# Kernel tuning notes

Hardware: AMD Instinct MI355X
Metric: run time of the kernel (lower is better)

The kernel has to match this reference:

```python
import jax, jax.numpy as jnp
import numpy as np

B, D, H = 8192, 1024, 1024

def setup_inputs() -> dict:
    key = jax.random.key(0)
    ks = jax.random.split(key, 7)
    s_x = 1.0 / np.sqrt(D)
    s_h = 1.0 / np.sqrt(H)
    return {
        "e_t": jax.random.normal(ks[0], (B, D), jnp.float32),
        "h_prev": jax.random.normal(ks[1], (B, H), jnp.float32),
        "c_prev": jax.random.normal(ks[2], (B, H), jnp.float32),
        # gates concatenated in order (f, i, o, c), each block of size H
        "W_x": jax.random.uniform(ks[3], (4 * H, D), jnp.float32, -s_x, s_x),
        "b_x": jax.random.uniform(ks[4], (4 * H,), jnp.float32, -s_x, s_x),
        "W_h": jax.random.uniform(ks[5], (4 * H, H), jnp.float32, -s_h, s_h),
        "b_h": jax.random.uniform(ks[6], (4 * H,), jnp.float32, -s_h, s_h),
        "b_extra": jnp.zeros((4 * H,), jnp.float32),  # the b_f/b_i/b_o/b_c Parameters
    }

def reference(e_t, h_prev, c_prev, W_x, b_x, W_h, b_h, b_extra):
    # two fused GEMMs: [B,D]@[D,4H] and [B,H]@[H,4H]
    z = (jnp.einsum('bd,gd->bg', e_t, W_x)
         + jnp.einsum('bh,gh->bg', h_prev, W_h)
         + b_x + b_h + b_extra)  # [B, 4H]
    zf, zi, zo, zc = jnp.split(z, 4, axis=-1)
    g_t = jax.nn.sigmoid(zf)   # forget gate
    p_t = jax.nn.sigmoid(zi)   # input gate
    q_t = jax.nn.sigmoid(zo)   # output gate
    m_t_hat = jnp.tanh(zc)     # candidate cell
    c_t = g_t * c_prev + p_t * m_t_hat
    h_t = q_t * jnp.tanh(c_t)
    return (h_t, c_t)
```

## Files before the change

kernel.cpp:

```cpp
#include <hip/hip_runtime.h>
#include <stdint.h>

#define B_ROWS 8192
#define DH     1024
#define KTOT   2048
#define NTOT   4096

typedef __attribute__((ext_vector_type(8))) __bf16 bf16x8;
typedef __attribute__((ext_vector_type(4))) float  f32x4;

__device__ __forceinline__ unsigned short f2bf(float f) {
    unsigned int u = __float_as_uint(f);
    u += 0x7FFFu + ((u >> 16) & 1u);
    return (unsigned short)(u >> 16);
}

__device__ __forceinline__ float fast_sigmoid(float x) {
    return 1.0f / (1.0f + __expf(-x));
}
__device__ __forceinline__ float fast_tanh(float x) {
    float e = __expf(fminf(-2.0f * x, 80.0f));
    return (1.0f - e) / (1.0f + e);
}
__device__ __forceinline__ float sel4(float g0, float g1, float g2, float g3, int u) {
    float r = g0;
    r = (u == 1) ? g1 : r;
    r = (u == 2) ? g2 : r;
    r = (u == 3) ? g3 : r;
    return r;
}

#define NBLK_A (B_ROWS)
#define NBLK_W (NTOT)
#define NBLK_BIAS (NTOT / 256)

__global__ __launch_bounds__(256) void pack_all(const float* __restrict__ e_t,
                                                const float* __restrict__ h_prev,
                                                const float* __restrict__ W_x,
                                                const float* __restrict__ W_h,
                                                const float* __restrict__ b_x,
                                                const float* __restrict__ b_h,
                                                const float* __restrict__ b_e,
                                                unsigned short* __restrict__ A_cat,
                                                unsigned short* __restrict__ W_cat,
                                                float* __restrict__ bias) {
    const int blk = blockIdx.x;
    const int t   = threadIdx.x;
    if (blk < NBLK_A + NBLK_W) {
        const float* src0;
        unsigned short* dst;
        int row;
        if (blk < NBLK_A) {
            row = blk;
            dst = A_cat + (size_t)row * KTOT;
            int c8 = t << 3;
            src0 = (c8 < DH) ? (e_t + (size_t)row * DH + c8)
                             : (h_prev + (size_t)row * DH + (c8 - DH));
        } else {
            row = blk - NBLK_A;
            int h = row >> 2, gate = row & 3;
            int srow = gate * DH + h;
            dst = W_cat + (size_t)row * KTOT;
            int c8 = t << 3;
            src0 = (c8 < DH) ? (W_x + (size_t)srow * DH + c8)
                             : (W_h + (size_t)srow * DH + (c8 - DH));
        }
        float4 f0 = ((const float4*)src0)[0];
        float4 f1 = ((const float4*)src0)[1];
        uint4 o;
        o.x = (unsigned)f2bf(f0.x) | ((unsigned)f2bf(f0.y) << 16);
        o.y = (unsigned)f2bf(f0.z) | ((unsigned)f2bf(f0.w) << 16);
        o.z = (unsigned)f2bf(f1.x) | ((unsigned)f2bf(f1.y) << 16);
        o.w = (unsigned)f2bf(f1.z) | ((unsigned)f2bf(f1.w) << 16);
        *(uint4*)(dst + t * 8) = o;
    } else {
        int gp = (blk - NBLK_A - NBLK_W) * 256 + t;
        int h = gp >> 2, gate = gp & 3;
        int g = gate * DH + h;
        bias[gp] = b_x[g] + b_h[g] + b_e[g];
    }
}


#define GLL(srcp, dstp) \
    __builtin_amdgcn_global_load_lds( \
        (const __attribute__((address_space(1))) void*)(srcp), \
        (__attribute__((address_space(3))) void*)(dstp), 16, 0, 0)

#define STAGE_HALF(g, buf, h, kt) do { \
    GLL((g) + ((size_t)((h) * 128)      * KTOT) + (size_t)(kt) * 64, (buf) + (((h) * 128)      + w8) * 128); \
    GLL((g) + ((size_t)((h) * 128 + 64) * KTOT) + (size_t)(kt) * 64, (buf) + (((h) * 128 + 64) + w8) * 128); \
} while (0)

#define PHASE_MID() do { \
    __builtin_amdgcn_sched_barrier(0); \
    __builtin_amdgcn_s_barrier(); \
    asm volatile("s_waitcnt lgkmcnt(0)" ::: "memory"); \
    __builtin_amdgcn_sched_barrier(0); \
} while (0)

#define PHASE_END() do { \
    __builtin_amdgcn_sched_barrier(0); \
    __builtin_amdgcn_s_barrier(); \
    __builtin_amdgcn_sched_barrier(0); \
} while (0)

template <int MODE>
__device__ __forceinline__ void do_tile(
    int kt,
    unsigned char* As_cur, unsigned char* Bs_cur,
    const unsigned short* __restrict__ gA, const unsigned short* __restrict__ gB,
    int w8, int rowA, int rowB, int xg0, int xg1,
    f32x4 (&acc)[8][4])
{
    bf16x8 afl[4][2], afh[4][2], bfl[2][2], bfh[2][2];

#pragma unroll
    for (int mi = 0; mi < 4; ++mi) {
        afl[mi][0] = *(const bf16x8*)(As_cur + rowA + mi * 2048 + xg0);
        afl[mi][1] = *(const bf16x8*)(As_cur + rowA + mi * 2048 + xg1);
    }
#pragma unroll
    for (int ni = 0; ni < 2; ++ni) {
        bfl[ni][0] = *(const bf16x8*)(Bs_cur + rowB + ni * 2048 + xg0);
        bfl[ni][1] = *(const bf16x8*)(Bs_cur + rowB + ni * 2048 + xg1);
    }
    PHASE_MID();
    __builtin_amdgcn_s_setprio(1);
#pragma unroll
    for (int mi = 0; mi < 4; ++mi)
#pragma unroll
        for (int ni = 0; ni < 2; ++ni) {
            acc[mi][ni] = __builtin_amdgcn_mfma_f32_16x16x32_bf16(afl[mi][0], bfl[ni][0], acc[mi][ni], 0, 0, 0);
            acc[mi][ni] = __builtin_amdgcn_mfma_f32_16x16x32_bf16(afl[mi][1], bfl[ni][1], acc[mi][ni], 0, 0, 0);
        }
    __builtin_amdgcn_s_setprio(0);
    PHASE_END();

#pragma unroll
    for (int ni = 0; ni < 2; ++ni) {
        bfh[ni][0] = *(const bf16x8*)(Bs_cur + rowB + (2 + ni) * 2048 + xg0);
        bfh[ni][1] = *(const bf16x8*)(Bs_cur + rowB + (2 + ni) * 2048 + xg1);
    }
    PHASE_MID();
    __builtin_amdgcn_s_setprio(1);
#pragma unroll
    for (int mi = 0; mi < 4; ++mi)
#pragma unroll
        for (int ni = 0; ni < 2; ++ni) {
            acc[mi][2 + ni] = __builtin_amdgcn_mfma_f32_16x16x32_bf16(afl[mi][0], bfh[ni][0], acc[mi][2 + ni], 0, 0, 0);
            acc[mi][2 + ni] = __builtin_amdgcn_mfma_f32_16x16x32_bf16(afl[mi][1], bfh[ni][1], acc[mi][2 + ni], 0, 0, 0);
        }
    __builtin_amdgcn_s_setprio(0);
    PHASE_END();

#pragma unroll
    for (int mi = 0; mi < 4; ++mi) {
        afh[mi][0] = *(const bf16x8*)(As_cur + rowA + (4 + mi) * 2048 + xg0);
        afh[mi][1] = *(const bf16x8*)(As_cur + rowA + (4 + mi) * 2048 + xg1);
    }
    if constexpr (MODE == 2) {
        STAGE_HALF(gB, Bs_cur, 0, kt + 2);
        STAGE_HALF(gB, Bs_cur, 1, kt + 2);
    }
    PHASE_MID();
    __builtin_amdgcn_s_setprio(1);
#pragma unroll
    for (int mi = 0; mi < 4; ++mi)
#pragma unroll
        for (int ni = 0; ni < 2; ++ni) {
            acc[4 + mi][ni] = __builtin_amdgcn_mfma_f32_16x16x32_bf16(afh[mi][0], bfl[ni][0], acc[4 + mi][ni], 0, 0, 0);
            acc[4 + mi][ni] = __builtin_amdgcn_mfma_f32_16x16x32_bf16(afh[mi][1], bfl[ni][1], acc[4 + mi][ni], 0, 0, 0);
        }
    __builtin_amdgcn_s_setprio(0);
    PHASE_END();

    if constexpr (MODE == 2) {
        STAGE_HALF(gA, As_cur, 0, kt + 2);
        STAGE_HALF(gA, As_cur, 1, kt + 2);
        __builtin_amdgcn_sched_barrier(0);
        asm volatile("s_waitcnt vmcnt(8)" ::: "memory");
        __builtin_amdgcn_sched_barrier(0);
    } else if constexpr (MODE == 1) {
        __builtin_amdgcn_sched_barrier(0);
        asm volatile("s_waitcnt vmcnt(0)" ::: "memory");
        __builtin_amdgcn_sched_barrier(0);
    }
    PHASE_MID();
    __builtin_amdgcn_s_setprio(1);
#pragma unroll
    for (int mi = 0; mi < 4; ++mi)
#pragma unroll
        for (int ni = 0; ni < 2; ++ni) {
            acc[4 + mi][2 + ni] = __builtin_amdgcn_mfma_f32_16x16x32_bf16(afh[mi][0], bfh[ni][0], acc[4 + mi][2 + ni], 0, 0, 0);
            acc[4 + mi][2 + ni] = __builtin_amdgcn_mfma_f32_16x16x32_bf16(afh[mi][1], bfh[ni][1], acc[4 + mi][2 + ni], 0, 0, 0);
        }
    __builtin_amdgcn_s_setprio(0);
    PHASE_END();
}

__global__ __launch_bounds__(512, 2) void lstm_gemm(
    const unsigned short* __restrict__ A,
    const unsigned short* __restrict__ Wc,
    const float* __restrict__ bias,
    const float* __restrict__ c_prev,
    float* __restrict__ h_out,
    float* __restrict__ c_out)
{
    __shared__ __align__(16) unsigned char lds[131072];

    const int tid = threadIdx.x;
    const int w   = tid >> 6;
    const int l   = tid & 63;
    const int wm  = w >> 2, wn = w & 3;
    const int m0  = blockIdx.y * 256;
    const int n0  = blockIdx.x * 256;
    const int w8  = w * 8;

    f32x4 acc[8][4];
#pragma unroll
    for (int i = 0; i < 8; ++i)
#pragma unroll
        for (int j = 0; j < 4; ++j) acc[i][j] = {0.f, 0.f, 0.f, 0.f};

    const int srow = w8 + (l >> 3);
    const int scol = ((l & 7) ^ ((l >> 3) & 7)) * 8;
    const unsigned short* gA = A  + (size_t)(m0 + srow) * KTOT + scol;
    const unsigned short* gB = Wc + (size_t)(n0 + srow) * KTOT + scol;

    unsigned char* As0 = lds;
    unsigned char* As1 = lds + 32768;
    unsigned char* Bs0 = lds + 65536;
    unsigned char* Bs1 = lds + 98304;

    const int lane15 = l & 15;
    const int quad   = l >> 4;
    const int rowA = (wm * 128 + lane15) * 128;
    const int rowB = (wn * 64  + lane15) * 128;
    const int xg0  = ((0 + quad) ^ (lane15 & 7)) * 16;
    const int xg1  = ((4 + quad) ^ (lane15 & 7)) * 16;

    STAGE_HALF(gA, As0, 0, 0);
    STAGE_HALF(gA, As0, 1, 0);
    STAGE_HALF(gB, Bs0, 0, 0);
    STAGE_HALF(gB, Bs0, 1, 0);
    STAGE_HALF(gA, As1, 0, 1);
    STAGE_HALF(gA, As1, 1, 1);
    STAGE_HALF(gB, Bs1, 0, 1);
    STAGE_HALF(gB, Bs1, 1, 1);
    asm volatile("s_waitcnt vmcnt(8)" ::: "memory");
    __builtin_amdgcn_s_barrier();

#pragma unroll 1
    for (int kt2 = 0; kt2 < 15; ++kt2) {
        do_tile<2>(2 * kt2,     As0, Bs0, gA, gB, w8, rowA, rowB, xg0, xg1, acc);
        do_tile<2>(2 * kt2 + 1, As1, Bs1, gA, gB, w8, rowA, rowB, xg0, xg1, acc);
    }
    do_tile<1>(30, As0, Bs0, gA, gB, w8, rowA, rowB, xg0, xg1, acc);
    do_tile<0>(31, As1, Bs1, gA, gB, w8, rowA, rowB, xg0, xg1, acc);

    float biasv[4];
#pragma unroll
    for (int nj = 0; nj < 4; ++nj)
        biasv[nj] = bias[n0 + wn * 64 + nj * 16 + lane15];

    const int u = (l >> 2) & 3;
    const int v = l & 3;
    const int src_base = (l & 0x30) | (v << 2);
    const int hbase = (n0 + wn * 64) >> 2;

#pragma unroll
    for (int mi = 0; mi < 8; ++mi) {
        const int m = m0 + wm * 128 + mi * 16 + quad * 4 + u;
#pragma unroll
        for (int nj = 0; nj < 4; ++nj) {
            f32x4 a = acc[mi][nj];
            float bb = biasv[nj];
            float a0 = a[0] + bb, a1 = a[1] + bb, a2 = a[2] + bb, a3 = a[3] + bb;

            float s0, s1, s2, s3;
            s0 = __shfl(a0, src_base | 0, 64); s1 = __shfl(a1, src_base | 0, 64);
            s2 = __shfl(a2, src_base | 0, 64); s3 = __shfl(a3, src_base | 0, 64);
            float zf = sel4(s0, s1, s2, s3, u);
            s0 = __shfl(a0, src_base | 1, 64); s1 = __shfl(a1, src_base | 1, 64);
            s2 = __shfl(a2, src_base | 1, 64); s3 = __shfl(a3, src_base | 1, 64);
            float zi = sel4(s0, s1, s2, s3, u);
            s0 = __shfl(a0, src_base | 2, 64); s1 = __shfl(a1, src_base | 2, 64);
            s2 = __shfl(a2, src_base | 2, 64); s3 = __shfl(a3, src_base | 2, 64);
            float zo = sel4(s0, s1, s2, s3, u);
            s0 = __shfl(a0, src_base | 3, 64); s1 = __shfl(a1, src_base | 3, 64);
            s2 = __shfl(a2, src_base | 3, 64); s3 = __shfl(a3, src_base | 3, 64);
            float zc = sel4(s0, s1, s2, s3, u);

            float gf = fast_sigmoid(zf);
            float gi = fast_sigmoid(zi);
            float go = fast_sigmoid(zo);
            float mh = fast_tanh(zc);

            const int h = hbase + nj * 4 + v;
            const size_t off = (size_t)m * DH + h;
            float cp = c_prev[off];
            float ct = gf * cp + gi * mh;
            float ht = go * fast_tanh(ct);
            h_out[off] = ht;
            c_out[off] = ct;
        }
    }
}

extern "C" void kernel_launch(void* const* d_in, const int* in_sizes, int n_in,
                              void* d_out, int out_size, void* d_ws, size_t ws_size,
                              hipStream_t stream) {
    const float* e_t     = (const float*)d_in[0];
    const float* h_prev  = (const float*)d_in[1];
    const float* c_prev  = (const float*)d_in[2];
    const float* W_x     = (const float*)d_in[3];
    const float* b_x     = (const float*)d_in[4];
    const float* W_h     = (const float*)d_in[5];
    const float* b_h     = (const float*)d_in[6];
    const float* b_extra = (const float*)d_in[7];

    float* h_out = (float*)d_out;
    float* c_out = h_out + (size_t)B_ROWS * DH;

    unsigned short* A_cat = (unsigned short*)d_ws;
    unsigned short* W_cat = (unsigned short*)((char*)d_ws + (size_t)B_ROWS * KTOT * 2);
    float*          bias  = (float*)((char*)d_ws + (size_t)B_ROWS * KTOT * 2 + (size_t)NTOT * KTOT * 2);

    pack_all<<<NBLK_A + NBLK_W + NBLK_BIAS, 256, 0, stream>>>(
        e_t, h_prev, W_x, W_h, b_x, b_h, b_extra, A_cat, W_cat, bias);
    lstm_gemm<<<dim3(NTOT / 256, B_ROWS / 256), 512, 0, stream>>>(
        A_cat, W_cat, bias, c_prev, h_out, c_out);
}
```

Baseline: 322.2 us.

## Regroup weight gate interleave by 16 and restructure LDS/MFMA phase synchronization

The packed weight and bias layout now interleaves gates in blocks of 16 columns instead of 4. Each lane's four accumulator fragments then hold f/i/o/c for the same hidden unit, so the epilogue's cross-lane shuffles and selects go away. The main loop issues all LDS fragment loads up front and uses counted lgkmcnt waits before each MFMA group. It also drops most of the per-phase workgroup barriers, keeping one before staging the next global-to-LDS loads and one at tile end. This cuts barrier stalls and shuffle overhead, at the risk of ordering hazards on reuse of the LDS buffers and higher register pressure.

```diff
diff --git a/kernel.cpp b/kernel.cpp
--- a/kernel.cpp
+++ b/kernel.cpp
@@ -21,13 +21,6 @@
 __device__ __forceinline__ float fast_tanh(float x) {
     float e = __expf(fminf(-2.0f * x, 80.0f));
     return (1.0f - e) / (1.0f + e);
-}
-__device__ __forceinline__ float sel4(float g0, float g1, float g2, float g3, int u) {
-    float r = g0;
-    r = (u == 1) ? g1 : r;
-    r = (u == 2) ? g2 : r;
-    r = (u == 3) ? g3 : r;
-    return r;
 }
 
 #define NBLK_A (B_ROWS)
@@ -58,7 +51,8 @@
                              : (h_prev + (size_t)row * DH + (c8 - DH));
         } else {
             row = blk - NBLK_A;
-            int h = row >> 2, gate = row & 3;
+            int gate = (row >> 4) & 3;
+            int h    = (row >> 6) * 16 + (row & 15);
             int srow = gate * DH + h;
             dst = W_cat + (size_t)row * KTOT;
             int c8 = t << 3;
@@ -75,8 +69,9 @@
         *(uint4*)(dst + t * 8) = o;
     } else {
         int gp = (blk - NBLK_A - NBLK_W) * 256 + t;
-        int h = gp >> 2, gate = gp & 3;
-        int g = gate * DH + h;
+        int gate = (gp >> 4) & 3;
+        int h    = (gp >> 6) * 16 + (gp & 15);
+        int g    = gate * DH + h;
         bias[gp] = b_x[g] + b_h[g] + b_e[g];
     }
 }
@@ -92,18 +87,7 @@
     GLL((g) + ((size_t)((h) * 128 + 64) * KTOT) + (size_t)(kt) * 64, (buf) + (((h) * 128 + 64) + w8) * 128); \
 } while (0)
 
-#define PHASE_MID() do { \
-    __builtin_amdgcn_sched_barrier(0); \
-    __builtin_amdgcn_s_barrier(); \
-    asm volatile("s_waitcnt lgkmcnt(0)" ::: "memory"); \
-    __builtin_amdgcn_sched_barrier(0); \
-} while (0)
-
-#define PHASE_END() do { \
-    __builtin_amdgcn_sched_barrier(0); \
-    __builtin_amdgcn_s_barrier(); \
-    __builtin_amdgcn_sched_barrier(0); \
-} while (0)
+#define SB() __builtin_amdgcn_sched_barrier(0)
 
 template <int MODE>
 __device__ __forceinline__ void do_tile(
@@ -125,7 +109,22 @@
         bfl[ni][0] = *(const bf16x8*)(Bs_cur + rowB + ni * 2048 + xg0);
         bfl[ni][1] = *(const bf16x8*)(Bs_cur + rowB + ni * 2048 + xg1);
     }
-    PHASE_MID();
+    SB();
+#pragma unroll
+    for (int ni = 0; ni < 2; ++ni) {
+        bfh[ni][0] = *(const bf16x8*)(Bs_cur + rowB + (2 + ni) * 2048 + xg0);
+        bfh[ni][1] = *(const bf16x8*)(Bs_cur + rowB + (2 + ni) * 2048 + xg1);
+    }
+    SB();
+#pragma unroll
+    for (int mi = 0; mi < 4; ++mi) {
+        afh[mi][0] = *(const bf16x8*)(As_cur + rowA + (4 + mi) * 2048 + xg0);
+        afh[mi][1] = *(const bf16x8*)(As_cur + rowA + (4 + mi) * 2048 + xg1);
+    }
+    SB();
+
+    asm volatile("s_waitcnt lgkmcnt(12)" ::: "memory");
+    SB();
     __builtin_amdgcn_s_setprio(1);
 #pragma unroll
     for (int mi = 0; mi < 4; ++mi)
@@ -135,14 +134,10 @@
             acc[mi][ni] = __builtin_amdgcn_mfma_f32_16x16x32_bf16(afl[mi][1], bfl[ni][1], acc[mi][ni], 0, 0, 0);
         }
     __builtin_amdgcn_s_setprio(0);
-    PHASE_END();
-
-#pragma unroll
-    for (int ni = 0; ni < 2; ++ni) {
-        bfh[ni][0] = *(const bf16x8*)(Bs_cur + rowB + (2 + ni) * 2048 + xg0);
-        bfh[ni][1] = *(const bf16x8*)(Bs_cur + rowB + (2 + ni) * 2048 + xg1);
-    }
-    PHASE_MID();
+    SB();
+
+    asm volatile("s_waitcnt lgkmcnt(8)" ::: "memory");
+    SB();
     __builtin_amdgcn_s_setprio(1);
 #pragma unroll
     for (int mi = 0; mi < 4; ++mi)
@@ -152,18 +147,20 @@
             acc[mi][2 + ni] = __builtin_amdgcn_mfma_f32_16x16x32_bf16(afl[mi][1], bfh[ni][1], acc[mi][2 + ni], 0, 0, 0);
         }
     __builtin_amdgcn_s_setprio(0);
-    PHASE_END();
-
-#pragma unroll
-    for (int mi = 0; mi < 4; ++mi) {
-        afh[mi][0] = *(const bf16x8*)(As_cur + rowA + (4 + mi) * 2048 + xg0);
-        afh[mi][1] = *(const bf16x8*)(As_cur + rowA + (4 + mi) * 2048 + xg1);
-    }
+    SB();
+
+    asm volatile("s_waitcnt lgkmcnt(0)" ::: "memory");
+    SB();
     if constexpr (MODE == 2) {
+        __builtin_amdgcn_s_barrier();
+        SB();
         STAGE_HALF(gB, Bs_cur, 0, kt + 2);
         STAGE_HALF(gB, Bs_cur, 1, kt + 2);
-    }
-    PHASE_MID();
+        STAGE_HALF(gA, As_cur, 0, kt + 2);
+        STAGE_HALF(gA, As_cur, 1, kt + 2);
+        SB();
+    }
+
     __builtin_amdgcn_s_setprio(1);
 #pragma unroll
     for (int mi = 0; mi < 4; ++mi)
@@ -173,20 +170,7 @@
             acc[4 + mi][ni] = __builtin_amdgcn_mfma_f32_16x16x32_bf16(afh[mi][1], bfl[ni][1], acc[4 + mi][ni], 0, 0, 0);
         }
     __builtin_amdgcn_s_setprio(0);
-    PHASE_END();
-
-    if constexpr (MODE == 2) {
-        STAGE_HALF(gA, As_cur, 0, kt + 2);
-        STAGE_HALF(gA, As_cur, 1, kt + 2);
-        __builtin_amdgcn_sched_barrier(0);
-        asm volatile("s_waitcnt vmcnt(8)" ::: "memory");
-        __builtin_amdgcn_sched_barrier(0);
-    } else if constexpr (MODE == 1) {
-        __builtin_amdgcn_sched_barrier(0);
-        asm volatile("s_waitcnt vmcnt(0)" ::: "memory");
-        __builtin_amdgcn_sched_barrier(0);
-    }
-    PHASE_MID();
+
     __builtin_amdgcn_s_setprio(1);
 #pragma unroll
     for (int mi = 0; mi < 4; ++mi)
@@ -196,7 +180,19 @@
             acc[4 + mi][2 + ni] = __builtin_amdgcn_mfma_f32_16x16x32_bf16(afh[mi][1], bfh[ni][1], acc[4 + mi][2 + ni], 0, 0, 0);
         }
     __builtin_amdgcn_s_setprio(0);
-    PHASE_END();
+    SB();
+
+    if constexpr (MODE == 2) {
+        asm volatile("s_waitcnt vmcnt(8)" ::: "memory");
+        SB();
+        __builtin_amdgcn_s_barrier();
+        SB();
+    } else if constexpr (MODE == 1) {
+        asm volatile("s_waitcnt vmcnt(0)" ::: "memory");
+        SB();
+        __builtin_amdgcn_s_barrier();
+        SB();
+    }
 }
 
 __global__ __launch_bounds__(512, 2) void lstm_gemm(
@@ -248,8 +244,11 @@
     STAGE_HALF(gA, As1, 1, 1);
     STAGE_HALF(gB, Bs1, 0, 1);
     STAGE_HALF(gB, Bs1, 1, 1);
+    SB();
     asm volatile("s_waitcnt vmcnt(8)" ::: "memory");
+    SB();
     __builtin_amdgcn_s_barrier();
+    SB();
 
 #pragma unroll 1
     for (int kt2 = 0; kt2 < 15; ++kt2) {
@@ -264,41 +263,28 @@
     for (int nj = 0; nj < 4; ++nj)
         biasv[nj] = bias[n0 + wn * 64 + nj * 16 + lane15];
 
-    const int u = (l >> 2) & 3;
-    const int v = l & 3;
-    const int src_base = (l & 0x30) | (v << 2);
-    const int hbase = (n0 + wn * 64) >> 2;
+    const int hcol = ((n0 + wn * 64) >> 6) * 16 + lane15;
 
 #pragma unroll
     for (int mi = 0; mi < 8; ++mi) {
-        const int m = m0 + wm * 128 + mi * 16 + quad * 4 + u;
-#pragma unroll
-        for (int nj = 0; nj < 4; ++nj) {
-            f32x4 a = acc[mi][nj];
-            float bb = biasv[nj];
-            float a0 = a[0] + bb, a1 = a[1] + bb, a2 = a[2] + bb, a3 = a[3] + bb;
-
-            float s0, s1, s2, s3;
-            s0 = __shfl(a0, src_base | 0, 64); s1 = __shfl(a1, src_base | 0, 64);
-            s2 = __shfl(a2, src_base | 0, 64); s3 = __shfl(a3, src_base | 0, 64);
-            float zf = sel4(s0, s1, s2, s3, u);
-            s0 = __shfl(a0, src_base | 1, 64); s1 = __shfl(a1, src_base | 1, 64);
-            s2 = __shfl(a2, src_base | 1, 64); s3 = __shfl(a3, src_base | 1, 64);
-            float zi = sel4(s0, s1, s2, s3, u);
-            s0 = __shfl(a0, src_base | 2, 64); s1 = __shfl(a1, src_base | 2, 64);
-            s2 = __shfl(a2, src_base | 2, 64); s3 = __shfl(a3, src_base | 2, 64);
-            float zo = sel4(s0, s1, s2, s3, u);
-            s0 = __shfl(a0, src_base | 3, 64); s1 = __shfl(a1, src_base | 3, 64);
-            s2 = __shfl(a2, src_base | 3, 64); s3 = __shfl(a3, src_base | 3, 64);
-            float zc = sel4(s0, s1, s2, s3, u);
+        const int mbase = m0 + wm * 128 + mi * 16 + quad * 4;
+        f32x4 zf4 = acc[mi][0];
+        f32x4 zi4 = acc[mi][1];
+        f32x4 zo4 = acc[mi][2];
+        f32x4 zc4 = acc[mi][3];
+#pragma unroll
+        for (int r = 0; r < 4; ++r) {
+            float zf = zf4[r] + biasv[0];
+            float zi = zi4[r] + biasv[1];
+            float zo = zo4[r] + biasv[2];
+            float zc = zc4[r] + biasv[3];
 
             float gf = fast_sigmoid(zf);
             float gi = fast_sigmoid(zi);
             float go = fast_sigmoid(zo);
             float mh = fast_tanh(zc);
 
-            const int h = hbase + nj * 4 + v;
-            const size_t off = (size_t)m * DH + h;
+            const size_t off = (size_t)(mbase + r) * DH + hcol;
             float cp = c_prev[off];
             float ct = gf * cp + gi * mh;
             float ht = go * fast_tanh(ct);
```

After: 295.7 us. -8.2%, faster.
